# Optimization experiments

Hardware: AMD Instinct MI355X
Metric: run time of the kernel (lower is better)

Reference implementation:

```python
import jax, jax.numpy as jnp
import numpy as np
import math

D_MODEL = 1024
N_HEADS = 16
D_HEAD = D_MODEL // N_HEADS
EPS = 1e-5


def layer_norm(x, w, b):
    mu = jnp.mean(x, axis=-1, keepdims=True)
    var = jnp.mean(jnp.square(x - mu), axis=-1, keepdims=True)
    return (x - mu) * jax.lax.rsqrt(var + EPS) * w + b


def setup_inputs() -> dict:
    key = jax.random.key(0)
    ks = jax.random.split(key, 8)
    b, n, d = 1, 4096, D_MODEL
    s = 0.02
    return {
        "x": jax.random.normal(ks[0], (b, n, d), dtype=jnp.float32),
        "ln1_w": jnp.ones((d,), jnp.float32),
        "ln1_b": jnp.zeros((d,), jnp.float32),
        "ln2_w": jnp.ones((d,), jnp.float32),
        "ln2_b": jnp.zeros((d,), jnp.float32),
        "w_qkv": jax.random.normal(ks[1], (d, 3 * d), jnp.float32) * s,  # [in, out]
        "w_o": jax.random.normal(ks[2], (d, d), jnp.float32) * s,
        "w_ff1": jax.random.normal(ks[3], (d, 4 * d), jnp.float32) * s,
        "b_ff1": jnp.zeros((4 * d,), jnp.float32),
        "w_ff2": jax.random.normal(ks[4], (4 * d, d), jnp.float32) * s,
        "b_ff2": jnp.zeros((d,), jnp.float32),
    }


def reference(x, ln1_w, ln1_b, ln2_w, ln2_b, w_qkv, w_o, w_ff1, b_ff1, w_ff2, b_ff2):
    b, n, d = x.shape
    # --- attention sub-block ---
    h = layer_norm(x, ln1_w, ln1_b)
    qkv = (h @ w_qkv).reshape(b, n, 3, N_HEADS, D_HEAD)
    q, k, v = qkv[:, :, 0], qkv[:, :, 1], qkv[:, :, 2]  # [b, n, h, dh]
    scale = 1.0 / math.sqrt(D_HEAD)
    s = jnp.einsum("bqhd,bkhd->bhqk", q, k) * scale  # materialized [b,h,n,n]
    causal = jnp.tril(jnp.ones((n, n), dtype=bool))
    s = jnp.where(causal, s, -jnp.inf)
    a = jax.nn.softmax(s, axis=-1)
    out = jnp.einsum("bhqk,bkhd->bqhd", a, v).reshape(b, n, d)
    x = x + out @ w_o
    # --- FFN sub-block ---
    h2 = layer_norm(x, ln2_w, ln2_b)
    ff = jax.nn.gelu(h2 @ w_ff1 + b_ff1, approximate=False) @ w_ff2 + b_ff2
    return x + ff
```

## Files before the change

### kernel.cpp

```cpp
#include <hip/hip_runtime.h>
#include <hip/hip_bf16.h>
#include <cstdint>
#include <cstddef>

typedef __attribute__((ext_vector_type(8))) __bf16 bf16x8;
typedef __attribute__((ext_vector_type(4))) __bf16 bf16x4;
typedef __attribute__((ext_vector_type(4))) float f32x4;
typedef __attribute__((ext_vector_type(16))) float f32x16;
typedef __attribute__((ext_vector_type(4))) unsigned int uint4v;

#define MFMA16(a, b, c) __builtin_amdgcn_mfma_f32_16x16x32_bf16(a, b, c, 0, 0, 0)
#define MFMA32(a, b, c) __builtin_amdgcn_mfma_f32_32x32x16_bf16(a, b, c, 0, 0, 0)

__device__ __forceinline__ void gload_lds16(const void* g, void* l) {
  __builtin_amdgcn_global_load_lds(
      (__attribute__((address_space(1))) uint32_t*)g,
      (__attribute__((address_space(3))) uint32_t*)l,
      16, 0, 0);
}

__device__ __forceinline__ unsigned pkbf(float a, float b) {
  unsigned short x = __builtin_bit_cast(unsigned short, (__bf16)a);
  unsigned short y = __builtin_bit_cast(unsigned short, (__bf16)b);
  return (unsigned)x | ((unsigned)y << 16);
}

__device__ __forceinline__ float fexp2(float x) {
  float r;
  asm("v_exp_f32 %0, %1" : "=v"(r) : "v"(x));
  return r;
}

__global__ __launch_bounds__(256) void pre_kernel(
    const float* __restrict__ w_qkv, __bf16* __restrict__ wqkvT,
    const float* __restrict__ x, const float* __restrict__ ln1_w,
    const float* __restrict__ ln1_b, __bf16* __restrict__ h) {
  __shared__ float sm[32 * 33];
  int bid = blockIdx.x;
  int tx = threadIdx.x, ty = threadIdx.y;
  if (bid < 3072) {
    int bx = bid % 96, by = bid / 96;
    int gcol = bx * 32 + tx;
#pragma unroll
    for (int j = 0; j < 4; j++) {
      int grow = by * 32 + ty + j * 8;
      sm[(ty + j * 8) * 33 + tx] = w_qkv[(size_t)grow * 3072 + gcol];
    }
    __syncthreads();
#pragma unroll
    for (int j = 0; j < 4; j++) {
      int n = bx * 32 + ty + j * 8;
      wqkvT[(size_t)n * 1024 + by * 32 + tx] = (__bf16)sm[tx * 33 + ty + j * 8];
    }
    return;
  }
  int row = bid - 3072;
  int t = ty * 32 + tx;
  const float4* xr = (const float4*)(x + (size_t)row * 1024);
  float4 v = xr[t];
  float s = v.x + v.y + v.z + v.w;
  float sq = v.x * v.x + v.y * v.y + v.z * v.z + v.w * v.w;
#pragma unroll
  for (int m = 1; m < 64; m <<= 1) {
    s += __shfl_xor(s, m);
    sq += __shfl_xor(sq, m);
  }
  float* rs = sm;
  float* rq = sm + 4;
  int wid = t >> 6;
  if ((t & 63) == 0) { rs[wid] = s; rq[wid] = sq; }
  __syncthreads();
  s = rs[0] + rs[1] + rs[2] + rs[3];
  sq = rq[0] + rq[1] + rq[2] + rq[3];
  float mean = s * (1.0f / 1024.0f);
  float var = sq * (1.0f / 1024.0f) - mean * mean;
  float rstd = rsqrtf(var + 1e-5f);
  float4 wv = ((const float4*)ln1_w)[t];
  float4 bv = ((const float4*)ln1_b)[t];
  bf16x4 o;
  o[0] = (__bf16)((v.x - mean) * rstd * wv.x + bv.x);
  o[1] = (__bf16)((v.y - mean) * rstd * wv.y + bv.y);
  o[2] = (__bf16)((v.z - mean) * rstd * wv.z + bv.z);
  o[3] = (__bf16)((v.w - mean) * rstd * wv.w + bv.w);
  *(bf16x4*)(h + (size_t)row * 1024 + t * 4) = o;
}

__global__ __launch_bounds__(256, 2) void gemm_splitk128_kernel(
    const __bf16* __restrict__ A, const __bf16* __restrict__ BT,
    int M, int N, int K, int kchunk, __bf16* __restrict__ P) {
  __shared__ __bf16 lsA[128 * 64];
  __shared__ __bf16 lsB[128 * 64];
  int t = threadIdx.x;
  int m0 = blockIdx.y * 128, n0 = blockIdx.x * 128;
  int kbase = blockIdx.z * kchunk;
  __bf16* pout = P + (size_t)blockIdx.z * M * N;
  int wid = t >> 6, lane = t & 63, lo = lane & 15, g = lane >> 4;
  int wr = wid >> 1, wc = wid & 1;
  f32x4 acc[4][4] = {};
  const __bf16* ag = A + (size_t)(m0 + (t >> 3)) * K + (t & 7) * 8;
  const __bf16* bg = BT + (size_t)(n0 + (t >> 3)) * K + (t & 7) * 8;
  for (int k0 = kbase; k0 < kbase + kchunk; k0 += 64) {
#pragma unroll
    for (int i = 0; i < 4; i++) {
      gload_lds16(ag + (size_t)i * 32 * K + k0, &lsA[i * 2048 + t * 8]);
      gload_lds16(bg + (size_t)i * 32 * K + k0, &lsB[i * 2048 + t * 8]);
    }
    __syncthreads();
#pragma unroll
    for (int kk = 0; kk < 2; kk++) {
      bf16x8 af[4], bfr[4];
#pragma unroll
      for (int mi = 0; mi < 4; mi++)
        af[mi] = *(const bf16x8*)&lsA[(wr * 64 + mi * 16 + lo) * 64 + kk * 32 + g * 8];
#pragma unroll
      for (int ni = 0; ni < 4; ni++)
        bfr[ni] = *(const bf16x8*)&lsB[(wc * 64 + ni * 16 + lo) * 64 + kk * 32 + g * 8];
#pragma unroll
      for (int mi = 0; mi < 4; mi++)
#pragma unroll
        for (int ni = 0; ni < 4; ni++)
          acc[mi][ni] = MFMA16(af[mi], bfr[ni], acc[mi][ni]);
    }
    __syncthreads();
  }
#pragma unroll
  for (int mi = 0; mi < 4; mi++) {
#pragma unroll
    for (int ni = 0; ni < 4; ni++) {
      int col = n0 + wc * 64 + ni * 16 + lo;
      int row0 = m0 + wr * 64 + mi * 16 + g * 4;
#pragma unroll
      for (int r = 0; r < 4; r++)
        pout[(size_t)(row0 + r) * N + col] = (__bf16)acc[mi][ni][r];
    }
  }
}

__global__ __launch_bounds__(256) void out_reduce_ln_kernel(
    const __bf16* __restrict__ p0, const __bf16* __restrict__ p1,
    const float* __restrict__ x, const float* __restrict__ w,
    const float* __restrict__ b, float* __restrict__ x2,
    __bf16* __restrict__ h) {
  int row = blockIdx.x, t = threadIdx.x;
  size_t base = (size_t)row * 1024 + t * 4;
  bf16x4 a = *(const bf16x4*)&p0[base];
  bf16x4 b4 = *(const bf16x4*)&p1[base];
  float4 xv = *(const float4*)&x[base];
  float4 v;
  v.x = xv.x + (float)a[0] + (float)b4[0];
  v.y = xv.y + (float)a[1] + (float)b4[1];
  v.z = xv.z + (float)a[2] + (float)b4[2];
  v.w = xv.w + (float)a[3] + (float)b4[3];
  *(float4*)&x2[base] = v;
  float s = v.x + v.y + v.z + v.w;
  float sq = v.x * v.x + v.y * v.y + v.z * v.z + v.w * v.w;
#pragma unroll
  for (int m = 1; m < 64; m <<= 1) {
    s += __shfl_xor(s, m);
    sq += __shfl_xor(sq, m);
  }
  __shared__ float rs[4], rq[4];
  int wid = t >> 6;
  if ((t & 63) == 0) { rs[wid] = s; rq[wid] = sq; }
  __syncthreads();
  s = rs[0] + rs[1] + rs[2] + rs[3];
  sq = rq[0] + rq[1] + rq[2] + rq[3];
  float mean = s * (1.0f / 1024.0f);
  float var = sq * (1.0f / 1024.0f) - mean * mean;
  float rstd = rsqrtf(var + 1e-5f);
  float4 wv = ((const float4*)w)[t];
  float4 bv = ((const float4*)b)[t];
  bf16x4 o;
  o[0] = (__bf16)((v.x - mean) * rstd * wv.x + bv.x);
  o[1] = (__bf16)((v.y - mean) * rstd * wv.y + bv.y);
  o[2] = (__bf16)((v.z - mean) * rstd * wv.z + bv.z);
  o[3] = (__bf16)((v.w - mean) * rstd * wv.w + bv.w);
  *(bf16x4*)&h[base] = o;
}

template <int EPI>
__global__ __launch_bounds__(512, 2) void gemm256_kernel(
    const __bf16* __restrict__ A, const __bf16* __restrict__ BT,
    int M, int N, int K, int nkc,
    const float* __restrict__ bias, __bf16* __restrict__ outb,
    __bf16* __restrict__ P0, __bf16* __restrict__ P1,
    __bf16* __restrict__ P2, __bf16* __restrict__ P3) {
  __shared__ __bf16 lsA[2][2][128 * 64];
  __shared__ __bf16 lsB[2][2][128 * 64];
  int nbx = N >> 8;
  int nwg = (M >> 8) * nbx;
  int bid = blockIdx.x;
  int swz = (bid & 7) * (nwg >> 3) + (bid >> 3);
  int m0 = (swz / nbx) << 8, n0 = (swz % nbx) << 8;
  int kc = blockIdx.y;
  int kt0 = kc * nkc;
  int t = threadIdx.x;
  int wid = t >> 6, lane = t & 63, lo = lane & 15, g = lane >> 4;
  int wm = wid >> 2, wn = wid & 3;
  int srow = t >> 3, sgrp = t & 7;

  auto stA = [&](int d, int h, int kt) {
#pragma unroll
    for (int i = 0; i < 2; i++) {
      int row = i * 64 + srow;
      int gs = (sgrp ^ (row & 7)) * 8;
      gload_lds16(A + (size_t)(m0 + h * 128 + row) * K + kt * 64 + gs,
                  &lsA[d][h][(i * 512 + t) * 8]);
    }
  };
  auto stB = [&](int d, int h, int kt) {
#pragma unroll
    for (int i = 0; i < 2; i++) {
      int row = i * 64 + srow;
      int gs = (sgrp ^ (row & 7)) * 8;
      gload_lds16(BT + (size_t)(n0 + h * 128 + row) * K + kt * 64 + gs,
                  &lsB[d][h][(i * 512 + t) * 8]);
    }
  };
  auto rdA = [&](int d, int f, int kk) -> bf16x8 {
    int row = (f & 3) * 32 + wm * 16 + lo;
    return *(const bf16x8*)&lsA[d][f >> 2][row * 64 + (((kk * 4 + g) ^ (lo & 7)) * 8)];
  };
  auto rdB = [&](int d, int ni, int kk) -> bf16x8 {
    int row = (ni & 1) * 64 + wn * 16 + lo;
    return *(const bf16x8*)&lsB[d][ni >> 1][row * 64 + (((kk * 4 + g) ^ (lo & 7)) * 8)];
  };

  f32x4 acc[8][4] = {};
  stA(0, 0, kt0); stB(0, 0, kt0); stB(0, 1, kt0); stA(0, 1, kt0);
  asm volatile("s_waitcnt vmcnt(4)" ::: "memory");
  __builtin_amdgcn_s_barrier();

  for (int ki = 0; ki < nkc; ki++) {
    int kt = kt0 + ki;
    int d = ki & 1, nx = d ^ 1;
    bool pf = (ki + 1) < nkc;
    bf16x8 fa[4][2], fb0[2][2], fb1[2][2];
#pragma unroll
    for (int f = 0; f < 4; f++) { fa[f][0] = rdA(d, f, 0); fa[f][1] = rdA(d, f, 1); }
#pragma unroll
    for (int n = 0; n < 2; n++) { fb0[n][0] = rdB(d, n, 0); fb0[n][1] = rdB(d, n, 1); }
    if (pf) { stA(nx, 0, kt + 1); stB(nx, 0, kt + 1); }
    __builtin_amdgcn_s_barrier();
    __builtin_amdgcn_s_setprio(1);
#pragma unroll
    for (int f = 0; f < 4; f++)
#pragma unroll
      for (int n = 0; n < 2; n++) {
        acc[f][n] = MFMA16(fa[f][0], fb0[n][0], acc[f][n]);
        acc[f][n] = MFMA16(fa[f][1], fb0[n][1], acc[f][n]);
      }
    __builtin_amdgcn_s_setprio(0);
    asm volatile("s_waitcnt vmcnt(6)" ::: "memory");
    __builtin_amdgcn_s_barrier();
#pragma unroll
    for (int n = 0; n < 2; n++) { fb1[n][0] = rdB(d, 2 + n, 0); fb1[n][1] = rdB(d, 2 + n, 1); }
    if (pf) stB(nx, 1, kt + 1);
    __builtin_amdgcn_s_barrier();
    __builtin_amdgcn_s_setprio(1);
#pragma unroll
    for (int f = 0; f < 4; f++)
#pragma unroll
      for (int n = 0; n < 2; n++) {
        acc[f][2 + n] = MFMA16(fa[f][0], fb1[n][0], acc[f][2 + n]);
        acc[f][2 + n] = MFMA16(fa[f][1], fb1[n][1], acc[f][2 + n]);
      }
    __builtin_amdgcn_s_setprio(0);
    asm volatile("s_waitcnt vmcnt(6)" ::: "memory");
    __builtin_amdgcn_s_barrier();
#pragma unroll
    for (int f = 0; f < 4; f++) { fa[f][0] = rdA(d, 4 + f, 0); fa[f][1] = rdA(d, 4 + f, 1); }
    if (pf) stA(nx, 1, kt + 1);
    __builtin_amdgcn_s_barrier();
    __builtin_amdgcn_s_setprio(1);
#pragma unroll
    for (int f = 0; f < 4; f++)
#pragma unroll
      for (int n = 0; n < 2; n++) {
        acc[4 + f][2 + n] = MFMA16(fa[f][0], fb1[n][0], acc[4 + f][2 + n]);
        acc[4 + f][2 + n] = MFMA16(fa[f][1], fb1[n][1], acc[4 + f][2 + n]);
      }
    __builtin_amdgcn_s_setprio(0);
    __builtin_amdgcn_s_barrier();
    __builtin_amdgcn_s_setprio(1);
#pragma unroll
    for (int f = 0; f < 4; f++)
#pragma unroll
      for (int n = 0; n < 2; n++) {
        acc[4 + f][n] = MFMA16(fa[f][0], fb0[n][0], acc[4 + f][n]);
        acc[4 + f][n] = MFMA16(fa[f][1], fb0[n][1], acc[4 + f][n]);
      }
    __builtin_amdgcn_s_setprio(0);
    asm volatile("s_waitcnt vmcnt(4)" ::: "memory");
    __builtin_amdgcn_s_barrier();
  }

  __bf16* pk = (EPI == 4) ? ((kc == 0) ? P0 : (kc == 1) ? P1 : (kc == 2) ? P2 : P3)
                          : nullptr;
#pragma unroll
  for (int f = 0; f < 8; f++) {
    int row0 = m0 + (f >> 2) * 128 + (f & 3) * 32 + wm * 16 + g * 4;
#pragma unroll
    for (int ni = 0; ni < 4; ni++) {
      int col = n0 + (ni >> 1) * 128 + (ni & 1) * 64 + wn * 16 + lo;
      if (EPI == 0) {
        int sE = col >> 10, rem = col & 1023, hh = rem >> 6, dd = rem & 63;
        if (sE < 2) {
          float qs = (sE == 0) ? 0.1803368801111204f : 1.0f;
#pragma unroll
          for (int r = 0; r < 4; r++)
            outb[((size_t)(sE * 16 + hh) * 4096 + row0 + r) * 64 + dd] =
                (__bf16)(acc[f][ni][r] * qs);
        } else {
          bf16x4 pk4;
#pragma unroll
          for (int r = 0; r < 4; r++) pk4[r] = (__bf16)acc[f][ni][r];
          *(bf16x4*)&outb[(size_t)32 * 4096 * 64 + ((size_t)(hh * 64 + dd)) * 4096 + row0] = pk4;
        }
      } else if (EPI == 2) {
        float bv = bias[col];
#pragma unroll
        for (int r = 0; r < 4; r++) {
          float vv = acc[f][ni][r] + bv;
          float gg = 0.5f * vv * (1.0f + erff(vv * 0.70710678118f));
          outb[(size_t)(row0 + r) * N + col] = (__bf16)gg;
        }
      } else {
#pragma unroll
        for (int r = 0; r < 4; r++)
          pk[(size_t)(row0 + r) * N + col] = (__bf16)acc[f][ni][r];
      }
    }
  }
}

__global__ __launch_bounds__(256) void ff2_reduce_kernel(
    const __bf16* __restrict__ p0, const __bf16* __restrict__ p1,
    const __bf16* __restrict__ p2, const __bf16* __restrict__ p3,
    const float* __restrict__ x2, const float* __restrict__ bias,
    float* __restrict__ out) {
  size_t i8 = ((size_t)blockIdx.x * 256 + threadIdx.x) * 8;
  bf16x8 a = *(const bf16x8*)&p0[i8];
  bf16x8 b = *(const bf16x8*)&p1[i8];
  bf16x8 c = *(const bf16x8*)&p2[i8];
  bf16x8 d = *(const bf16x8*)&p3[i8];
  int col = (int)(i8 & 1023);
  float4 xa = *(const float4*)&x2[i8];
  float4 xb = *(const float4*)&x2[i8 + 4];
  float4 ba = *(const float4*)&bias[col];
  float4 bb = *(const float4*)&bias[col + 4];
  float4 oa, ob;
  oa.x = xa.x + ba.x + (float)a[0] + (float)b[0] + (float)c[0] + (float)d[0];
  oa.y = xa.y + ba.y + (float)a[1] + (float)b[1] + (float)c[1] + (float)d[1];
  oa.z = xa.z + ba.z + (float)a[2] + (float)b[2] + (float)c[2] + (float)d[2];
  oa.w = xa.w + ba.w + (float)a[3] + (float)b[3] + (float)c[3] + (float)d[3];
  ob.x = xb.x + bb.x + (float)a[4] + (float)b[4] + (float)c[4] + (float)d[4];
  ob.y = xb.y + bb.y + (float)a[5] + (float)b[5] + (float)c[5] + (float)d[5];
  ob.z = xb.z + bb.z + (float)a[6] + (float)b[6] + (float)c[6] + (float)d[6];
  ob.w = xb.w + bb.w + (float)a[7] + (float)b[7] + (float)c[7] + (float)d[7];
  *(float4*)&out[i8] = oa;
  *(float4*)&out[i8 + 4] = ob;
}

__global__ __launch_bounds__(256) void attn_merge_kernel(
    const __bf16* __restrict__ pO, const float* __restrict__ pL,
    __bf16* __restrict__ attnb) {
  size_t i8 = ((size_t)blockIdx.x * 256 + threadIdx.x) * 8;
  int row = (int)(i8 >> 10);
  int col = (int)(i8 & 1023);
  int head = col >> 6, d = col & 63;
  size_t po_off = (((size_t)head * 4096) + row) * 64 + d;
  bf16x8 a = *(const bf16x8*)&pO[po_off];
  bf16x8 b = *(const bf16x8*)&pO[(size_t)16 * 4096 * 64 + po_off];
  float l0 = pL[(size_t)head * 4096 + row];
  float l1 = pL[(size_t)16 * 4096 + (size_t)head * 4096 + row];
  float linv = 1.0f / (l0 + l1);
  bf16x8 o;
#pragma unroll
  for (int i = 0; i < 8; i++)
    o[i] = (__bf16)(((float)a[i] + (float)b[i]) * linv);
  *(bf16x8*)&attnb[i8] = o;
}

__global__ __launch_bounds__(256, 4) void attn_fused_kernel(
    const __bf16* __restrict__ Q, const __bf16* __restrict__ Kb,
    const __bf16* __restrict__ VTb, __bf16* __restrict__ pO,
    float* __restrict__ pL,
    const float* __restrict__ w_o, __bf16* __restrict__ woT,
    const float* __restrict__ w_ff1, __bf16* __restrict__ wff1T,
    const float* __restrict__ w_ff2, __bf16* __restrict__ wff2T) {
  constexpr int NSEQ = 4096;
  __shared__ __bf16 lds[2][2][64 * 64];
  int orig = blockIdx.x;
  int t = threadIdx.x;

  if (orig >= 1024) {
    int b = orig - 1024;
    const float* in; __bf16* outw; int K, N, bx, by;
    if (b < 1024)      { in = w_o;   outw = woT;   K = 1024; N = 1024; bx = b & 31;  by = b >> 5; }
    else if (b < 5120) { int c = b - 1024; in = w_ff1; outw = wff1T; K = 1024; N = 4096; bx = c & 127; by = c >> 7; }
    else               { int c = b - 5120; in = w_ff2; outw = wff2T; K = 4096; N = 1024; bx = c & 31;  by = c >> 5; }
    float* tile = (float*)lds;
    int tx = t & 31, ty = t >> 5;
#pragma unroll
    for (int j = 0; j < 4; j++) {
      int r = ty + j * 8;
      tile[r * 33 + tx] = in[(size_t)(by * 32 + r) * N + bx * 32 + tx];
    }
    __syncthreads();
#pragma unroll
    for (int j = 0; j < 4; j++) {
      int r = ty + j * 8;
      outw[(size_t)(bx * 32 + r) * K + by * 32 + tx] = (__bf16)tile[tx * 33 + r];
    }
    return;
  }

  int xcd = orig & 7, r = orig >> 3;
  int kpar = r & 1;
  int r2 = r >> 1;
  int hv = r2 >> 5;
  int hd2 = (r2 >> 4) & 1;
  int itr = r2 & 15;
  int head = xcd * 2 + hd2;
  int it = hv ? itr : (31 - itr);
  int wid = t >> 6, lane = t & 63;
  int lo = lane & 31, hi = lane >> 5;
  int qsub = wid;
  const __bf16* kh = Kb + (size_t)head * NSEQ * 64;
  const __bf16* vth = VTb + (size_t)head * 64 * NSEQ;
  int qlow = it * 128 + qsub * 32;
  int qrow = qlow + lo;
  int qtop = qlow + 31;
  const __bf16* qh = Q + (size_t)head * NSEQ * 64 + (size_t)qrow * 64;
  bf16x8 bq[4];
#pragma unroll
  for (int c = 0; c < 4; c++) bq[c] = *(const bf16x8*)(qh + c * 16 + hi * 8);

  const unsigned onesu = 0x3F803F80u;
  uint4v onev = {onesu, onesu, onesu, onesu};
  bf16x8 vones = __builtin_bit_cast(bf16x8, onev);

  f32x16 acc0 = {}, acc1 = {};
  f32x16 lacc = {};
  int srow = t >> 3;
  int sgs = ((t & 7) ^ (srow & 7)) * 8;

  int off[4];
#pragma unroll
  for (int c = 0; c < 4; c++) off[c] = lo * 64 + (((c * 2 + hi) ^ (lo & 7)) * 8);
  const __bf16* lk0 = &lds[0][0][0];
  const __bf16* lk1 = &lds[1][0][0];
  const __bf16* lv0 = &lds[0][1][0];
  const __bf16* lv1 = &lds[1][1][0];
  const __bf16* khs = kh + srow * 64 + sgs;
  const __bf16* vts = vth + (size_t)srow * NSEQ + sgs;

  auto stage_tile = [&](int d, int kt) {
#pragma unroll
    for (int i = 0; i < 2; i++) {
      gload_lds16(khs + (size_t)kt * 4096 + i * 2048, &lds[d][0][i * 2048 + t * 8]);
      gload_lds16(vts + (size_t)i * 32 * NSEQ + kt * 64, &lds[d][1][i * 2048 + t * 8]);
    }
  };

  int ns = it + 1;
  stage_tile(0, kpar);
  __syncthreads();

#define ATTN_STEP(CUR)                                                         \
  {                                                                            \
    int kt = 2 * j + kpar;                                                     \
    if (j + 1 < ns) stage_tile((CUR) ^ 1, kt + 2);                             \
    if (kt * 64 <= qtop) {                                                     \
      const __bf16* lk = (CUR) ? lk1 : lk0;                                    \
      const __bf16* lvt = (CUR) ? lv1 : lv0;                                   \
      f32x16 s0 = {}, s1 = {};                                                 \
      __builtin_amdgcn_s_setprio(1);                                           \
      _Pragma("unroll") for (int c = 0; c < 4; c++) {                          \
        bf16x8 ka0 = *(const bf16x8*)&lk[off[c]];                              \
        bf16x8 ka1 = *(const bf16x8*)&lk[2048 + off[c]];                       \
        s0 = MFMA32(ka0, bq[c], s0);                                           \
        s1 = MFMA32(ka1, bq[c], s1);                                           \
      }                                                                        \
      __builtin_amdgcn_s_setprio(0);                                           \
      if (kt * 64 + 63 > qlow) {                                               \
        _Pragma("unroll") for (int i = 0; i < 16; i++) {                       \
          int key0 = kt * 64 + (i & 3) + 8 * (i >> 2) + 4 * hi;                \
          if (key0 > qrow) s0[i] = -3.0e38f;                                   \
          if (key0 + 32 > qrow) s1[i] = -3.0e38f;                              \
        }                                                                      \
      }                                                                        \
      _Pragma("unroll") for (int i = 0; i < 16; i++) {                         \
        s0[i] = fexp2(s0[i]);                                                  \
        s1[i] = fexp2(s1[i]);                                                  \
      }                                                                        \
      uint4v pw[4];                                                            \
      _Pragma("unroll") for (int b = 0; b < 2; b++) {                          \
        int off2 = b * 8;                                                      \
        unsigned a0 = pkbf(s0[off2 + 0], s0[off2 + 1]);                        \
        unsigned a1 = pkbf(s0[off2 + 2], s0[off2 + 3]);                        \
        unsigned b0 = pkbf(s0[off2 + 4], s0[off2 + 5]);                        \
        unsigned b1 = pkbf(s0[off2 + 6], s0[off2 + 7]);                        \
        asm("v_permlane32_swap_b32 %0, %1" : "+v"(a0), "+v"(b0));              \
        asm("v_permlane32_swap_b32 %0, %1" : "+v"(a1), "+v"(b1));              \
        pw[b][0] = a0; pw[b][1] = a1; pw[b][2] = b0; pw[b][3] = b1;            \
        unsigned c0 = pkbf(s1[off2 + 0], s1[off2 + 1]);                        \
        unsigned c1 = pkbf(s1[off2 + 2], s1[off2 + 3]);                        \
        unsigned d0 = pkbf(s1[off2 + 4], s1[off2 + 5]);                        \
        unsigned d1 = pkbf(s1[off2 + 6], s1[off2 + 7]);                        \
        asm("v_permlane32_swap_b32 %0, %1" : "+v"(c0), "+v"(d0));              \
        asm("v_permlane32_swap_b32 %0, %1" : "+v"(c1), "+v"(d1));              \
        pw[2 + b][0] = c0; pw[2 + b][1] = c1; pw[2 + b][2] = d0;               \
        pw[2 + b][3] = d1;                                                     \
      }                                                                        \
      __builtin_amdgcn_s_setprio(1);                                           \
      _Pragma("unroll") for (int b = 0; b < 4; b++) {                          \
        bf16x8 pf = __builtin_bit_cast(bf16x8, pw[b]);                         \
        bf16x8 va0 = *(const bf16x8*)&lvt[off[b]];                             \
        bf16x8 va1 = *(const bf16x8*)&lvt[2048 + off[b]];                      \
        acc0 = MFMA32(va0, pf, acc0);                                          \
        acc1 = MFMA32(va1, pf, acc1);                                          \
        lacc = MFMA32(vones, pf, lacc);                                        \
      }                                                                        \
      __builtin_amdgcn_s_setprio(0);                                           \
    }                                                                          \
    __syncthreads();                                                           \
  }

  int j = 0;
  for (;;) {
    ATTN_STEP(0);
    if (++j >= ns) break;
    ATTN_STEP(1);
    if (++j >= ns) break;
  }
#undef ATTN_STEP

  if (hi == 0) pL[((size_t)kpar * 16 + head) * 4096 + qlow + lo] = lacc[0];
  __bf16* bounce = (__bf16*)lds;
  __bf16* region = bounce + qsub * 2048;
#pragma unroll
  for (int dt = 0; dt < 2; dt++) {
#pragma unroll
    for (int rp = 0; rp < 8; rp++) {
      int rr = rp * 2;
      float e0 = dt ? acc1[rr] : acc0[rr];
      float e1 = dt ? acc1[rr + 1] : acc0[rr + 1];
      int d = dt * 32 + (rr & 3) + 8 * (rr >> 2) + 4 * hi;
      int bytecol = d * 2;
      int g16 = bytecol >> 4, rem16 = bytecol & 15;
      *(unsigned*)((char*)region + lo * 128 + ((g16 ^ (lo & 7)) * 16 + rem16)) = pkbf(e0, e1);
    }
  }
  __syncthreads();
  __bf16* pok = pO + (size_t)kpar * 16 * 4096 * 64 + (((size_t)head * 4096) + qlow) * 64;
#pragma unroll
  for (int j2 = 0; j2 < 4; j2++) {
    int idx = j2 * 64 + lane;
    int row = idx >> 3, g = idx & 7;
    bf16x8 v = *(const bf16x8*)((char*)region + row * 128 + ((g ^ (row & 7)) * 16));
    *(bf16x8*)&pok[(size_t)row * 64 + g * 8] = v;
  }
}

extern "C" void kernel_launch(void* const* d_in, const int* in_sizes, int n_in,
                              void* d_out, int out_size, void* d_ws, size_t ws_size,
                              hipStream_t stream) {
  const float* x = (const float*)d_in[0];
  const float* ln1_w = (const float*)d_in[1];
  const float* ln1_b = (const float*)d_in[2];
  const float* ln2_w = (const float*)d_in[3];
  const float* ln2_b = (const float*)d_in[4];
  const float* w_qkv = (const float*)d_in[5];
  const float* w_o = (const float*)d_in[6];
  const float* w_ff1 = (const float*)d_in[7];
  const float* b_ff1 = (const float*)d_in[8];
  const float* w_ff2 = (const float*)d_in[9];
  const float* b_ff2 = (const float*)d_in[10];
  float* out = (float*)d_out;

  const size_t D = 1024, NT = 4096;
  __bf16* wqkvT = (__bf16*)d_ws;
  __bf16* woT = wqkvT + 3072 * D;
  __bf16* wff1T = woT + D * D;
  __bf16* wff2T = wff1T + 4096 * D;
  __bf16* hbuf = wff2T + D * 4096;
  __bf16* qkvb = hbuf + NT * D;
  __bf16* attnb = qkvb + 3 * NT * D;
  __bf16* a1 = qkvb;
  float* x2 = (float*)(attnb + NT * D);
  __bf16* p0 = (__bf16*)d_ws;
  __bf16* p1 = p0 + NT * D;
  __bf16* p2 = hbuf;
  __bf16* p3 = (__bf16*)(x2 + NT * D);
  __bf16* pA = qkvb;
  __bf16* pB = pA + NT * D;
  __bf16* pOb = (__bf16*)x2;
  float* pLb = (float*)p3;

  dim3 tb(32, 8);
  pre_kernel<<<3072 + 4096, tb, 0, stream>>>(w_qkv, wqkvT, x, ln1_w, ln1_b, hbuf);
  gemm256_kernel<0><<<192, 512, 0, stream>>>(hbuf, wqkvT, 4096, 3072, 1024, 16,
                                             nullptr, qkvb, nullptr, nullptr, nullptr, nullptr);
  attn_fused_kernel<<<1024 + 9216, 256, 0, stream>>>(
      qkvb, qkvb + 16 * NT * 64, qkvb + 32 * NT * 64, pOb, pLb,
      w_o, woT, w_ff1, wff1T, w_ff2, wff2T);
  attn_merge_kernel<<<2048, 256, 0, stream>>>(pOb, pLb, attnb);
  gemm_splitk128_kernel<<<dim3(8, 32, 2), 256, 0, stream>>>(
      attnb, woT, 4096, 1024, 1024, 512, pA);
  out_reduce_ln_kernel<<<4096, 256, 0, stream>>>(pA, pB, x, ln2_w, ln2_b, x2, hbuf);
  gemm256_kernel<2><<<256, 512, 0, stream>>>(hbuf, wff1T, 4096, 4096, 1024, 16,
                                             b_ff1, a1, nullptr, nullptr, nullptr, nullptr);
  gemm256_kernel<4><<<dim3(64, 4), 512, 0, stream>>>(a1, wff2T, 4096, 1024, 4096, 16,
                                                     nullptr, nullptr, p0, p1, p2, p3);
  ff2_reduce_kernel<<<2048, 256, 0, stream>>>(p0, p1, p2, p3, x2, b_ff2, out);
}
```

Measured before the change: 231.9 us.

## Drop attention key-split and merge kernel; normalize output in-kernel

Attention no longer splits each query tile's keys into two parity halves across separate blocks. Each block now walks all key tiles itself, normalizes by the softmax denominator, and writes the final bf16 output directly in row-major layout, so the separate merge kernel and its partial-output traffic go away. The cost is half as many attention blocks, each with a serial key loop twice as long. That lowers parallelism and lengthens the critical path for the largest causal tiles.

```diff
diff --git a/kernel.cpp b/kernel.cpp
--- a/kernel.cpp
+++ b/kernel.cpp
@@ -362,30 +362,9 @@
   *(float4*)&out[i8 + 4] = ob;
 }
 
-__global__ __launch_bounds__(256) void attn_merge_kernel(
-    const __bf16* __restrict__ pO, const float* __restrict__ pL,
-    __bf16* __restrict__ attnb) {
-  size_t i8 = ((size_t)blockIdx.x * 256 + threadIdx.x) * 8;
-  int row = (int)(i8 >> 10);
-  int col = (int)(i8 & 1023);
-  int head = col >> 6, d = col & 63;
-  size_t po_off = (((size_t)head * 4096) + row) * 64 + d;
-  bf16x8 a = *(const bf16x8*)&pO[po_off];
-  bf16x8 b = *(const bf16x8*)&pO[(size_t)16 * 4096 * 64 + po_off];
-  float l0 = pL[(size_t)head * 4096 + row];
-  float l1 = pL[(size_t)16 * 4096 + (size_t)head * 4096 + row];
-  float linv = 1.0f / (l0 + l1);
-  bf16x8 o;
-#pragma unroll
-  for (int i = 0; i < 8; i++)
-    o[i] = (__bf16)(((float)a[i] + (float)b[i]) * linv);
-  *(bf16x8*)&attnb[i8] = o;
-}
-
 __global__ __launch_bounds__(256, 4) void attn_fused_kernel(
     const __bf16* __restrict__ Q, const __bf16* __restrict__ Kb,
-    const __bf16* __restrict__ VTb, __bf16* __restrict__ pO,
-    float* __restrict__ pL,
+    const __bf16* __restrict__ VTb, __bf16* __restrict__ O,
     const float* __restrict__ w_o, __bf16* __restrict__ woT,
     const float* __restrict__ w_ff1, __bf16* __restrict__ wff1T,
     const float* __restrict__ w_ff2, __bf16* __restrict__ wff2T) {
@@ -394,8 +373,8 @@
   int orig = blockIdx.x;
   int t = threadIdx.x;
 
-  if (orig >= 1024) {
-    int b = orig - 1024;
+  if (orig >= 512) {
+    int b = orig - 512;
     const float* in; __bf16* outw; int K, N, bx, by;
     if (b < 1024)      { in = w_o;   outw = woT;   K = 1024; N = 1024; bx = b & 31;  by = b >> 5; }
     else if (b < 5120) { int c = b - 1024; in = w_ff1; outw = wff1T; K = 1024; N = 4096; bx = c & 127; by = c >> 7; }
@@ -416,9 +395,7 @@
     return;
   }
 
-  int xcd = orig & 7, r = orig >> 3;
-  int kpar = r & 1;
-  int r2 = r >> 1;
+  int xcd = orig & 7, r2 = orig >> 3;
   int hv = r2 >> 5;
   int hd2 = (r2 >> 4) & 1;
   int itr = r2 & 15;
@@ -464,15 +441,15 @@
     }
   };
 
-  int ns = it + 1;
-  stage_tile(0, kpar);
+  int nt = 2 * it + 2;
+  stage_tile(0, 0);
   __syncthreads();
 
 #define ATTN_STEP(CUR)                                                         \
   {                                                                            \
-    int kt = 2 * j + kpar;                                                     \
-    if (j + 1 < ns) stage_tile((CUR) ^ 1, kt + 2);                             \
-    if (kt * 64 <= qtop) {                                                     \
+    if (j + 1 < nt) stage_tile((CUR) ^ 1, j + 1);                              \
+    if (j * 64 <= qtop) {                                                      \
+      int kt = j;                                                              \
       const __bf16* lk = (CUR) ? lk1 : lk0;                                    \
       const __bf16* lvt = (CUR) ? lv1 : lv0;                                   \
       f32x16 s0 = {}, s1 = {};                                                 \
@@ -531,13 +508,13 @@
   int j = 0;
   for (;;) {
     ATTN_STEP(0);
-    if (++j >= ns) break;
+    if (++j >= nt) break;
     ATTN_STEP(1);
-    if (++j >= ns) break;
+    if (++j >= nt) break;
   }
 #undef ATTN_STEP
 
-  if (hi == 0) pL[((size_t)kpar * 16 + head) * 4096 + qlow + lo] = lacc[0];
+  float linv = 1.0f / lacc[0];
   __bf16* bounce = (__bf16*)lds;
   __bf16* region = bounce + qsub * 2048;
 #pragma unroll
@@ -545,8 +522,8 @@
 #pragma unroll
     for (int rp = 0; rp < 8; rp++) {
       int rr = rp * 2;
-      float e0 = dt ? acc1[rr] : acc0[rr];
-      float e1 = dt ? acc1[rr + 1] : acc0[rr + 1];
+      float e0 = (dt ? acc1[rr] : acc0[rr]) * linv;
+      float e1 = (dt ? acc1[rr + 1] : acc0[rr + 1]) * linv;
       int d = dt * 32 + (rr & 3) + 8 * (rr >> 2) + 4 * hi;
       int bytecol = d * 2;
       int g16 = bytecol >> 4, rem16 = bytecol & 15;
@@ -554,13 +531,12 @@
     }
   }
   __syncthreads();
-  __bf16* pok = pO + (size_t)kpar * 16 * 4096 * 64 + (((size_t)head * 4096) + qlow) * 64;
 #pragma unroll
   for (int j2 = 0; j2 < 4; j2++) {
     int idx = j2 * 64 + lane;
     int row = idx >> 3, g = idx & 7;
     bf16x8 v = *(const bf16x8*)((char*)region + row * 128 + ((g ^ (row & 7)) * 16));
-    *(bf16x8*)&pok[(size_t)row * 64 + g * 8] = v;
+    *(bf16x8*)&O[(size_t)(it * 128 + qsub * 32 + row) * 1024 + head * 64 + g * 8] = v;
   }
 }
 
@@ -596,17 +572,14 @@
   __bf16* p3 = (__bf16*)(x2 + NT * D);
   __bf16* pA = qkvb;
   __bf16* pB = pA + NT * D;
-  __bf16* pOb = (__bf16*)x2;
-  float* pLb = (float*)p3;
 
   dim3 tb(32, 8);
   pre_kernel<<<3072 + 4096, tb, 0, stream>>>(w_qkv, wqkvT, x, ln1_w, ln1_b, hbuf);
   gemm256_kernel<0><<<192, 512, 0, stream>>>(hbuf, wqkvT, 4096, 3072, 1024, 16,
                                              nullptr, qkvb, nullptr, nullptr, nullptr, nullptr);
-  attn_fused_kernel<<<1024 + 9216, 256, 0, stream>>>(
-      qkvb, qkvb + 16 * NT * 64, qkvb + 32 * NT * 64, pOb, pLb,
+  attn_fused_kernel<<<512 + 9216, 256, 0, stream>>>(
+      qkvb, qkvb + 16 * NT * 64, qkvb + 32 * NT * 64, attnb,
       w_o, woT, w_ff1, wff1T, w_ff2, wff2T);
-  attn_merge_kernel<<<2048, 256, 0, stream>>>(pOb, pLb, attnb);
   gemm_splitk128_kernel<<<dim3(8, 32, 2), 256, 0, stream>>>(
       attnb, woT, 4096, 1024, 1024, 512, pA);
   out_reduce_ln_kernel<<<4096, 256, 0, stream>>>(pA, pB, x, ln2_w, ln2_b, x2, hbuf);
```

New measurement: 233.5 us. No clear change (+0.7%).
